# Performance work log

Hardware: AMD Instinct MI355X
Metric: run time of the kernel (lower is better)

Reference implementation:

```python
import jax, jax.numpy as jnp
import numpy as np

B, N, H = 4, 4096, 256

def setup_inputs() -> dict:
    key = jax.random.key(0)
    ks = jax.random.split(key, 7)
    s = 1.0 / np.sqrt(H)
    return {
        "x": jax.random.normal(ks[0], (B, N, H), dtype=jnp.float32),
        "Wq": jax.random.uniform(ks[1], (H, H), jnp.float32, -s, s),
        "bq": jax.random.uniform(ks[2], (H,), jnp.float32, -s, s),
        "Wk": jax.random.uniform(ks[3], (H, H), jnp.float32, -s, s),
        "bk": jax.random.uniform(ks[4], (H,), jnp.float32, -s, s),
        "Wv": jax.random.uniform(ks[5], (H, H), jnp.float32, -s, s),
        "bv": jax.random.uniform(ks[6], (H,), jnp.float32, -s, s),
    }

def reference(x, Wq, bq, Wk, bk, Wv, bv):
    # torch Linear: y = x @ W.T + b
    q = jnp.einsum('bnh,oh->bno', x, Wq) + bq
    k = jnp.einsum('bnh,oh->bno', x, Wk) + bk
    v = jnp.einsum('bnh,oh->bno', x, Wv) + bv
    # NOTE: original module does NOT scale by 1/sqrt(d)
    scores = jnp.einsum('bik,bjk->bij', q, k)          # [B, N, N]
    attention = jax.nn.softmax(scores, axis=-1)
    attended = jnp.einsum('bij,bjk->bik', attention, v)  # [B, N, H]
    return attended
```

## Files before the change

### kernel.cpp

```cpp
#include <hip/hip_runtime.h>

#define B_ 4
#define N_ 4096
#define H_ 256
#define BN_ (B_*N_)
#define L2E 1.44269504088896340736f

typedef _Float16 f16;
typedef __fp16 fp16x2 __attribute__((ext_vector_type(2)));
typedef f16 f16x4 __attribute__((ext_vector_type(4)));
typedef f16 f16x8 __attribute__((ext_vector_type(8)));
typedef float f32x4 __attribute__((ext_vector_type(4)));
typedef float f32x16 __attribute__((ext_vector_type(16)));
typedef unsigned u32x2 __attribute__((ext_vector_type(2)));

static __device__ __forceinline__ f32x16 mfma32(f16x8 a, f16x8 b, f32x16 c){
  return __builtin_amdgcn_mfma_f32_32x32x16_f16(a, b, c, 0, 0, 0);
}
static __device__ __forceinline__ unsigned pkrtz(float a, float b){
  fp16x2 h = __builtin_amdgcn_cvt_pkrtz(a, b);
  return __builtin_bit_cast(unsigned, h);
}
static __device__ __forceinline__ u32x2 pls(unsigned a, unsigned b){
#if __has_builtin(__builtin_amdgcn_permlane32_swap)
  return __builtin_amdgcn_permlane32_swap(a, b, false, false);
#else
  asm volatile("v_permlane32_swap_b32 %0, %1" : "+v"(a), "+v"(b));
  u32x2 r; r[0] = a; r[1] = b; return r;
#endif
}
static __device__ __forceinline__ u32x2 plsf(float a, float b){
  return pls(__builtin_bit_cast(unsigned, a), __builtin_bit_cast(unsigned, b));
}
static __device__ __forceinline__ float asf(unsigned u){
  return __builtin_bit_cast(float, u);
}

static __device__ __forceinline__ void gload16(const void* g, void* l){
  __builtin_amdgcn_global_load_lds(
    (const __attribute__((address_space(1))) unsigned int*)g,
    (__attribute__((address_space(3))) unsigned int*)l, 16, 0, 0);
}

static __device__ __forceinline__ f16x8 cvt8(const float* __restrict__ p){
  float4 f0 = *(const float4*)p, f1 = *(const float4*)(p + 4);
  f16x8 v;
  v[0]=(f16)f0.x; v[1]=(f16)f0.y; v[2]=(f16)f0.z; v[3]=(f16)f0.w;
  v[4]=(f16)f1.x; v[5]=(f16)f1.y; v[6]=(f16)f1.z; v[7]=(f16)f1.w;
  return v;
}

__global__ __launch_bounds__(256) void cvt_w_frag(
    const float* __restrict__ W0, const float* __restrict__ W1,
    const float* __restrict__ W2, f16* __restrict__ Wf){
  int u = blockIdx.x * 256 + threadIdx.x;
  int m = u >> 13, u13 = u & 8191;
  const float* W = (m == 0) ? W0 : ((m == 1) ? W1 : W2);
  int ol = u13 & 31, t = u13 >> 5;
  int hi = t & 1, ks = (t >> 1) & 15, ot = t >> 5;
  int o = ot*32 + ol;
  *(f16x8*)(Wf + (size_t)u * 8) = cvt8(W + o*256 + ks*16 + hi*8);
}

__global__ __launch_bounds__(512, 2) void proj_qkv(
    const float* __restrict__ X, const f16* __restrict__ Wf,
    const float* __restrict__ bq, const float* __restrict__ bk,
    const float* __restrict__ bv,
    f16* __restrict__ Yq, f16* __restrict__ Yk, f16* __restrict__ Yvt){
  __shared__ f16 Xl[64*256];
  const int tid = threadIdx.x, l = tid & 63, w = tid >> 6;
  const int ol = l & 31, hi = l >> 5;
  const int m0 = blockIdx.x * 64;

  #pragma unroll
  for (int i = 0; i < 4; ++i){
    int c = i*512 + tid;
    int r = c >> 5, x = c & 31;
    f16x8 v = cvt8(X + (size_t)(m0 + r)*H_ + ((x ^ (r & 7)) << 3));
    *(f16x8*)(Xl + (size_t)c*8) = v;
  }
  __syncthreads();

  f32x16 aq[2], ak[2], av[2];
  #pragma unroll
  for (int ms = 0; ms < 2; ++ms)
    #pragma unroll
    for (int e = 0; e < 16; ++e){ aq[ms][e]=0.f; ak[ms][e]=0.f; av[ms][e]=0.f; }

  const char* Xb = (const char*)Xl;
  #pragma unroll
  for (int ks = 0; ks < 16; ++ks){
    int cw = ks*2 + hi;
    f16x8 a0 = *(const f16x8*)(Xb + ((     ol)*32 + (cw ^ (ol & 7))) * 16);
    f16x8 a1 = *(const f16x8*)(Xb + ((32 + ol)*32 + (cw ^ (ol & 7))) * 16);
    size_t wu = ((size_t)((w*16 + ks)*2 + hi))*256 + ol*8;
    f16x8 wqf = *(const f16x8*)(Wf + wu);
    f16x8 wkf = *(const f16x8*)(Wf + 65536 + wu);
    f16x8 wvf = *(const f16x8*)(Wf + 131072 + wu);
    aq[0] = mfma32(a0, wqf, aq[0]);  aq[1] = mfma32(a1, wqf, aq[1]);
    ak[0] = mfma32(a0, wkf, ak[0]);  ak[1] = mfma32(a1, wkf, ak[1]);
    av[0] = mfma32(a0, wvf, av[0]);  av[1] = mfma32(a1, wvf, av[1]);
  }

  const int o = w*32 + ol;
  const float Bq = bq[o], Bk = bk[o], Bv = bv[o];
  const int bb = m0 >> 12;
  const int nn0 = m0 & (N_-1);
  #pragma unroll
  for (int ms = 0; ms < 2; ++ms){
    #pragma unroll
    for (int rg = 0; rg < 4; ++rg){
      int rbase = m0 + ms*32 + 8*rg + 4*hi;
      f16x4 pk;
      #pragma unroll
      for (int j = 0; j < 4; ++j){
        float vq = (ms ? aq[1][4*rg+j] : aq[0][4*rg+j]) + Bq;
        float vk = (ms ? ak[1][4*rg+j] : ak[0][4*rg+j]) + Bk;
        float vv = (ms ? av[1][4*rg+j] : av[0][4*rg+j]) + Bv;
        Yq[(size_t)(rbase + j)*H_ + o] = (f16)vq;
        Yk[(size_t)(rbase + j)*H_ + o] = (f16)vk;
        pk[j] = (f16)vv;
      }
      *(f16x4*)(Yvt + ((size_t)(bb*H_ + o))*N_ + nn0 + ms*32 + 8*rg + 4*hi) = pk;
    }
  }
}

__global__ __launch_bounds__(512, 2) void flash_kernel(
    const f16* __restrict__ Q, const f16* __restrict__ K,
    const f16* __restrict__ Vt, f16* __restrict__ Opn, float* __restrict__ mll){
  __shared__ __align__(16) char lds[132*1024];
  f16* Kl0 = (f16*)lds;
  f16* Vl0 = (f16*)(lds + 65536);
  float* mlb = (float*)(lds + 131072);

  const int tid = threadIdx.x, l = tid & 63, w = tid >> 6;
  const int q32 = l & 31, hi = l >> 5;
  const int strip = w & 3, kvh = w >> 2;
  const int qblk = blockIdx.x >> 1, kb = blockIdx.x & 1;
  const int b = qblk >> 5, qt = qblk & 31;
  const int q0 = qt * 128;
  const int kvbase = kb * 2048;
  const f16* Kg = K  + (size_t)b * N_ * H_;
  const f16* Vg = Vt + (size_t)b * H_ * N_;

  f16x8 qf[16];
  {
    const f16* qp = Q + ((size_t)b*N_ + q0 + strip*32 + q32) * H_ + hi*8;
    #pragma unroll
    for (int ks = 0; ks < 16; ++ks) qf[ks] = *(const f16x8*)(qp + ks*16);
  }

  f32x16 oacc[8];
  #pragma unroll
  for (int ft = 0; ft < 8; ++ft)
    #pragma unroll
    for (int e = 0; e < 16; ++e) oacc[ft][e] = 0.f;
  float m_run = -3.0e38f, l_run = 0.f;

  auto stage = [&](int buf, int t){
    const int kv0 = kvbase + t * 64;
    #pragma unroll
    for (int i = 0; i < 4; ++i){
      int c = i*512 + tid;
      int r = c >> 5, x = c & 31;
      gload16(Kg + (size_t)(kv0 + r)*H_ + ((x ^ (r & 7)) << 3),
              Kl0 + buf*16384 + (i*512 + (tid & ~63)) * 8);
    }
    #pragma unroll
    for (int i = 0; i < 4; ++i){
      int c = i*512 + tid;
      int f = c >> 3, x = c & 7;
      gload16(Vg + (size_t)f*N_ + kv0 + ((x ^ (f & 7)) << 3),
              Vl0 + buf*16384 + (i*512 + (tid & ~63)) * 8);
    }
  };

  stage(0, 0);
  __syncthreads();

  const int krow = kvh*32 + q32;
  for (int t = 0; t < 32; ++t){
    const int cur = t & 1;
    if (t + 1 < 32) stage(cur ^ 1, t + 1);

    f32x16 s;
    #pragma unroll
    for (int e = 0; e < 16; ++e) s[e] = 0.f;
    const char* Kb = (const char*)(Kl0 + cur*16384);
    __builtin_amdgcn_s_setprio(1);
    #pragma unroll
    for (int ks = 0; ks < 16; ++ks){
      int cw = ks*2 + hi;
      f16x8 ka = *(const f16x8*)(Kb + krow*512 + ((cw ^ (krow & 7)) << 4));
      s = mfma32(ka, qf[ks], s);
    }
    __builtin_amdgcn_s_setprio(0);

    float m8[8];
    #pragma unroll
    for (int e = 0; e < 8; ++e) m8[e] = fmaxf(s[e], s[e+8]);
    #pragma unroll
    for (int e = 0; e < 4; ++e) m8[e] = fmaxf(m8[e], m8[e+4]);
    float mloc = fmaxf(fmaxf(m8[0], m8[2]), fmaxf(m8[1], m8[3]));
    u32x2 mr = plsf(mloc, mloc);
    float mx = fmaxf(asf(mr[0]), asf(mr[1]));
    if (!__all(mx - m_run <= 8.0f)){
      float mn = fmaxf(m_run, mx);
      float al = __builtin_amdgcn_exp2f((m_run - mn) * L2E);
      m_run = mn; l_run *= al;
      #pragma unroll
      for (int ft = 0; ft < 8; ++ft)
        #pragma unroll
        for (int e = 0; e < 16; ++e) oacc[ft][e] *= al;
    }
    #pragma unroll
    for (int e = 0; e < 16; ++e)
      s[e] = __builtin_amdgcn_exp2f((s[e] - m_run) * L2E);
    float p8[8];
    #pragma unroll
    for (int e = 0; e < 8; ++e) p8[e] = s[e] + s[e+8];
    #pragma unroll
    for (int e = 0; e < 4; ++e) p8[e] = p8[e] + p8[e+4];
    float ps = (p8[0] + p8[2]) + (p8[1] + p8[3]);
    u32x2 pr = plsf(ps, ps);
    l_run += asf(pr[0]) + asf(pr[1]);

    unsigned xw[4], yw[4];
    #pragma unroll
    for (int o = 0; o < 4; ++o){
      xw[o] = pkrtz(s[4*o],   s[4*o+1]);
      yw[o] = pkrtz(s[4*o+2], s[4*o+3]);
    }

    const char* Vb = (const char*)(Vl0 + cur*16384);
    #pragma unroll
    for (int ks2 = 0; ks2 < 2; ++ks2){
      u32x2 r0 = pls(xw[2*ks2], xw[2*ks2+1]);
      u32x2 r1 = pls(yw[2*ks2], yw[2*ks2+1]);
      union { unsigned u[4]; f16x8 v; } pa;
      pa.u[0] = r0[0];
      pa.u[1] = r1[0];
      pa.u[2] = r0[1];
      pa.u[3] = r1[1];
      __builtin_amdgcn_s_setprio(1);
      #pragma unroll
      for (int ft = 0; ft < 8; ++ft){
        int f  = ft*32 + q32;
        int cw = kvh*4 + ks2*2 + hi;
        f16x8 va = *(const f16x8*)(Vb + f*128 + ((cw ^ (f & 7)) << 4));
        oacc[ft] = mfma32(va, pa.v, oacc[ft]);
      }
      __builtin_amdgcn_s_setprio(0);
    }
    __syncthreads();
  }

  __syncthreads();
  float* scr = (float*)lds;
  if (kvh == 1){
    #pragma unroll
    for (int ft = 0; ft < 8; ++ft)
      #pragma unroll
      for (int rg = 0; rg < 4; ++rg){
        int c = 8*ft + 2*rg + hi;
        f32x4 v = { oacc[ft][4*rg], oacc[ft][4*rg+1],
                    oacc[ft][4*rg+2], oacc[ft][4*rg+3] };
        *(f32x4*)(scr + strip*8192 + q32*256 + (c ^ (q32 & 7))*4) = v;
      }
    if (hi == 0){ mlb[strip*32 + q32] = m_run; mlb[128 + strip*32 + q32] = l_run; }
  }
  __syncthreads();
  if (kvh == 0){
    float mB = mlb[strip*32 + q32], lB = mlb[128 + strip*32 + q32];
    float mM = fmaxf(m_run, mB);
    float e0 = __builtin_amdgcn_exp2f((m_run - mM) * L2E);
    float e1 = __builtin_amdgcn_exp2f((mB    - mM) * L2E);
    float lM = e0*l_run + e1*lB;
    float inv = 1.0f / lM;
    size_t row = (size_t)b*N_ + q0 + strip*32 + q32;
    f16* od = Opn + ((size_t)kb*BN_ + row) * H_;
    #pragma unroll
    for (int ft = 0; ft < 8; ++ft)
      #pragma unroll
      for (int rg = 0; rg < 4; ++rg){
        int c = 8*ft + 2*rg + hi;
        f32x4 vB = *(const f32x4*)(scr + strip*8192 + q32*256 + (c ^ (q32 & 7))*4);
        f16x4 hv;
        #pragma unroll
        for (int j = 0; j < 4; ++j)
          hv[j] = (f16)((e0*oacc[ft][4*rg+j] + e1*vB[j]) * inv);
        *(f16x4*)(od + 32*ft + 8*rg + 4*hi) = hv;
      }
    if (hi == 0) mll[(size_t)kb*BN_ + row] = mM*L2E + __log2f(lM);
  }
}

__global__ __launch_bounds__(256) void merge_kernel(
    const f16* __restrict__ Opn, const float* __restrict__ mll,
    float* __restrict__ out){
  int i = blockIdx.x*256 + threadIdx.x;
  int row = i >> 6, c = i & 63;
  float g0 = mll[row], g1 = mll[BN_ + row];
  float gm = fmaxf(g0, g1);
  float w0 = __builtin_amdgcn_exp2f(g0 - gm);
  float w1 = __builtin_amdgcn_exp2f(g1 - gm);
  float inv = 1.0f / (w0 + w1);
  f16x4 a  = *(const f16x4*)(Opn + (size_t)row*H_ + c*4);
  f16x4 bq = *(const f16x4*)(Opn + ((size_t)BN_ + row)*H_ + c*4);
  float4 o;
  o.x = (w0*(float)a[0] + w1*(float)bq[0]) * inv;
  o.y = (w0*(float)a[1] + w1*(float)bq[1]) * inv;
  o.z = (w0*(float)a[2] + w1*(float)bq[2]) * inv;
  o.w = (w0*(float)a[3] + w1*(float)bq[3]) * inv;
  *(float4*)(out + (size_t)row*H_ + c*4) = o;
}

extern "C" void kernel_launch(void* const* d_in, const int* in_sizes, int n_in,
                              void* d_out, int out_size, void* d_ws, size_t ws_size,
                              hipStream_t stream) {
  const float* x  = (const float*)d_in[0];
  const float* Wq = (const float*)d_in[1];
  const float* bq = (const float*)d_in[2];
  const float* Wk = (const float*)d_in[3];
  const float* bk = (const float*)d_in[4];
  const float* Wv = (const float*)d_in[5];
  const float* bv = (const float*)d_in[6];
  float* out = (float*)d_out;

  char* ws = (char*)d_ws;
  const size_t SZ = (size_t)BN_ * H_ * 2;
  f16*   qb  = (f16*)(ws);
  f16*   kb  = (f16*)(ws + SZ);
  f16*   vt  = (f16*)(ws + 2*SZ);
  f16*   opn = (f16*)(ws + 3*SZ);
  float* mll = (float*)(ws + 5*SZ);
  f16*   wf  = (f16*)(ws + 5*SZ + 131072);

  cvt_w_frag<<<96, 256, 0, stream>>>(Wq, Wk, Wv, wf);
  proj_qkv<<<BN_/64, 512, 0, stream>>>(x, wf, bq, bk, bv, qb, kb, vt);
  flash_kernel<<<(BN_/128)*2, 512, 0, stream>>>(qb, kb, vt, opn, mll);
  merge_kernel<<<BN_*64/256, 256, 0, stream>>>(opn, mll, out);
}
```

Before: 121.4 us.

## Interleave K/V prefetch with MFMA phases using explicit waitcnt and barriers

Splits the next tile's K and V global-to-LDS staging into per-phase chunks and issues them interleaved with the QK and PV MFMA phases. Replaces __syncthreads with fine-grained vmcnt/lgkmcnt waits and s_barrier ping-pong so K can be consumed while V is still in flight. The aim is to hide global load latency behind matrix work and to coordinate waves in lockstep. In exchange it adds many more workgroup barriers per iteration and depends on exact vmcnt accounting being correct.

```diff
diff --git a/kernel.cpp b/kernel.cpp
--- a/kernel.cpp
+++ b/kernel.cpp
@@ -150,6 +150,8 @@
     #pragma unroll
     for (int ks = 0; ks < 16; ++ks) qf[ks] = *(const f16x8*)(qp + ks*16);
   }
+  asm volatile("s_waitcnt vmcnt(0)" ::: "memory");
+  __builtin_amdgcn_sched_barrier(0);
 
   f32x16 oacc[8];
   #pragma unroll
@@ -158,44 +160,69 @@
     for (int e = 0; e < 16; ++e) oacc[ft][e] = 0.f;
   float m_run = -3.0e38f, l_run = 0.f;
 
-  auto stage = [&](int buf, int t){
+  auto stageK = [&](int buf, int t, int i){
     const int kv0 = kvbase + t * 64;
-    #pragma unroll
-    for (int i = 0; i < 4; ++i){
-      int c = i*512 + tid;
-      int r = c >> 5, x = c & 31;
-      gload16(Kg + (size_t)(kv0 + r)*H_ + ((x ^ (r & 7)) << 3),
-              Kl0 + buf*16384 + (i*512 + (tid & ~63)) * 8);
-    }
-    #pragma unroll
-    for (int i = 0; i < 4; ++i){
-      int c = i*512 + tid;
-      int f = c >> 3, x = c & 7;
-      gload16(Vg + (size_t)f*N_ + kv0 + ((x ^ (f & 7)) << 3),
-              Vl0 + buf*16384 + (i*512 + (tid & ~63)) * 8);
-    }
+    int c = i*512 + tid;
+    int r = c >> 5, x = c & 31;
+    gload16(Kg + (size_t)(kv0 + r)*H_ + ((x ^ (r & 7)) << 3),
+            Kl0 + buf*16384 + (i*512 + (tid & ~63)) * 8);
   };
-
-  stage(0, 0);
-  __syncthreads();
+  auto stageV = [&](int buf, int t, int i){
+    const int kv0 = kvbase + t * 64;
+    int c = i*512 + tid;
+    int f = c >> 3, x = c & 7;
+    gload16(Vg + (size_t)f*N_ + kv0 + ((x ^ (f & 7)) << 3),
+            Vl0 + buf*16384 + (i*512 + (tid & ~63)) * 8);
+  };
+
+  #pragma unroll
+  for (int i = 0; i < 4; ++i) stageK(0, 0, i);
+  #pragma unroll
+  for (int i = 0; i < 4; ++i) stageV(0, 0, i);
 
   const int krow = kvh*32 + q32;
   for (int t = 0; t < 32; ++t){
-    const int cur = t & 1;
-    if (t + 1 < 32) stage(cur ^ 1, t + 1);
+    const int cur = t & 1, nxt = cur ^ 1;
+    const bool more = (t + 1 < 32);
+    const char* Kb = (const char*)(Kl0 + cur*16384);
+    const char* Vb = (const char*)(Vl0 + cur*16384);
+
+    asm volatile("s_waitcnt vmcnt(4)" ::: "memory");
+    __builtin_amdgcn_sched_barrier(0);
+    __builtin_amdgcn_s_barrier();
 
     f32x16 s;
     #pragma unroll
     for (int e = 0; e < 16; ++e) s[e] = 0.f;
-    const char* Kb = (const char*)(Kl0 + cur*16384);
-    __builtin_amdgcn_s_setprio(1);
-    #pragma unroll
-    for (int ks = 0; ks < 16; ++ks){
-      int cw = ks*2 + hi;
-      f16x8 ka = *(const f16x8*)(Kb + krow*512 + ((cw ^ (krow & 7)) << 4));
-      s = mfma32(ka, qf[ks], s);
-    }
-    __builtin_amdgcn_s_setprio(0);
+    #pragma unroll
+    for (int ph = 0; ph < 4; ++ph){
+      f16x8 k0, k1, k2, k3;
+      {
+        const int c0 = (ph*4+0)*2 + hi, c1 = (ph*4+1)*2 + hi;
+        const int c2 = (ph*4+2)*2 + hi, c3 = (ph*4+3)*2 + hi;
+        const int xr = krow & 7;
+        k0 = *(const f16x8*)(Kb + krow*512 + ((c0 ^ xr) << 4));
+        k1 = *(const f16x8*)(Kb + krow*512 + ((c1 ^ xr) << 4));
+        k2 = *(const f16x8*)(Kb + krow*512 + ((c2 ^ xr) << 4));
+        k3 = *(const f16x8*)(Kb + krow*512 + ((c3 ^ xr) << 4));
+      }
+      if (more){
+        if (ph < 2){ stageK(nxt, t+1, 2*ph);     stageK(nxt, t+1, 2*ph+1); }
+        else       { stageV(nxt, t+1, 2*(ph-2)); stageV(nxt, t+1, 2*(ph-2)+1); }
+      }
+      __builtin_amdgcn_sched_barrier(0);
+      __builtin_amdgcn_s_barrier();
+      asm volatile("s_waitcnt lgkmcnt(0)" ::: "memory");
+      __builtin_amdgcn_sched_barrier(0);
+      __builtin_amdgcn_s_setprio(1);
+      s = mfma32(k0, qf[ph*4+0], s);
+      s = mfma32(k1, qf[ph*4+1], s);
+      s = mfma32(k2, qf[ph*4+2], s);
+      s = mfma32(k3, qf[ph*4+3], s);
+      __builtin_amdgcn_s_setprio(0);
+      __builtin_amdgcn_sched_barrier(0);
+      __builtin_amdgcn_s_barrier();
+    }
 
     float m8[8];
     #pragma unroll
@@ -233,7 +260,11 @@
       yw[o] = pkrtz(s[4*o+2], s[4*o+3]);
     }
 
-    const char* Vb = (const char*)(Vl0 + cur*16384);
+    if (t == 31){ asm volatile("s_waitcnt vmcnt(0)" ::: "memory"); }
+    else        { asm volatile("s_waitcnt vmcnt(8)" ::: "memory"); }
+    __builtin_amdgcn_sched_barrier(0);
+    __builtin_amdgcn_s_barrier();
+
     #pragma unroll
     for (int ks2 = 0; ks2 < 2; ++ks2){
       u32x2 r0 = pls(xw[2*ks2], xw[2*ks2+1]);
@@ -243,17 +274,32 @@
       pa.u[1] = r1[0];
       pa.u[2] = r0[1];
       pa.u[3] = r1[1];
-      __builtin_amdgcn_s_setprio(1);
-      #pragma unroll
-      for (int ft = 0; ft < 8; ++ft){
-        int f  = ft*32 + q32;
-        int cw = kvh*4 + ks2*2 + hi;
-        f16x8 va = *(const f16x8*)(Vb + f*128 + ((cw ^ (f & 7)) << 4));
-        oacc[ft] = mfma32(va, pa.v, oacc[ft]);
-      }
-      __builtin_amdgcn_s_setprio(0);
-    }
-    __syncthreads();
+      #pragma unroll
+      for (int hf = 0; hf < 2; ++hf){
+        f16x8 v0, v1, v2, v3;
+        {
+          const int cw = kvh*4 + ks2*2 + hi;
+          const int f0 = (hf*4+0)*32 + q32, f1 = (hf*4+1)*32 + q32;
+          const int f2 = (hf*4+2)*32 + q32, f3 = (hf*4+3)*32 + q32;
+          v0 = *(const f16x8*)(Vb + f0*128 + ((cw ^ (f0 & 7)) << 4));
+          v1 = *(const f16x8*)(Vb + f1*128 + ((cw ^ (f1 & 7)) << 4));
+          v2 = *(const f16x8*)(Vb + f2*128 + ((cw ^ (f2 & 7)) << 4));
+          v3 = *(const f16x8*)(Vb + f3*128 + ((cw ^ (f3 & 7)) << 4));
+        }
+        __builtin_amdgcn_sched_barrier(0);
+        __builtin_amdgcn_s_barrier();
+        asm volatile("s_waitcnt lgkmcnt(0)" ::: "memory");
+        __builtin_amdgcn_sched_barrier(0);
+        __builtin_amdgcn_s_setprio(1);
+        oacc[hf*4+0] = mfma32(v0, pa.v, oacc[hf*4+0]);
+        oacc[hf*4+1] = mfma32(v1, pa.v, oacc[hf*4+1]);
+        oacc[hf*4+2] = mfma32(v2, pa.v, oacc[hf*4+2]);
+        oacc[hf*4+3] = mfma32(v3, pa.v, oacc[hf*4+3]);
+        __builtin_amdgcn_s_setprio(0);
+        __builtin_amdgcn_sched_barrier(0);
+        __builtin_amdgcn_s_barrier();
+      }
+    }
   }
 
   __syncthreads();
```

Result: slower. 147.5 us (+21.6%).
